# Kernel optimization log

Hardware: AMD Instinct MI355X
Metric: run time of the kernel (lower is better)

## Reference

```python
import jax, jax.numpy as jnp
import numpy as np

N_NODES = 100000
N_EDGES = 1600000
D_IN = 128
D_OUT = 128


def setup_inputs() -> dict:
    key = jax.random.key(0)
    k1, k2, k3, k4, k5, k6 = jax.random.split(key, 6)
    x = jax.random.normal(k1, (N_NODES, D_IN), dtype=jnp.float32)
    row = jnp.sort(jax.random.randint(k2, (N_EDGES,), 0, N_NODES, dtype=jnp.int32))
    col = jax.random.randint(k3, (N_EDGES,), 0, N_NODES, dtype=jnp.int32)
    val = jax.random.uniform(k4, (N_EDGES,), dtype=jnp.float32)
    # Glorot init for the two linear weights (stored as [in, out] for x @ W)
    std_l = float(np.sqrt(6.0 / (D_IN + D_OUT)))
    W_l = jax.random.uniform(k5, (D_IN, D_OUT), minval=-std_l, maxval=std_l, dtype=jnp.float32)
    b_l = jnp.zeros((D_OUT,), dtype=jnp.float32)
    W_r = jax.random.uniform(k6, (D_IN, D_OUT), minval=-std_l, maxval=std_l, dtype=jnp.float32)
    return {"x": x, "row": row, "col": col, "val": val, "W_l": W_l, "b_l": b_l, "W_r": W_r}


def reference(x, row, col, val, W_l, b_l, W_r):
    n = x.shape[0]
    # out_l = graph @ x  (sparse COO matmul: gather source feats, scale, scatter-add to rows)
    msg = val[:, None] * x[col]                      # [E, D_in]
    out_l = jax.ops.segment_sum(msg, row, num_segments=n)  # [N, D_in]
    # lin_l(out_l) + lin_r(x)
    return out_l @ W_l + b_l + x @ W_r
```

## Files before the change

kernel.cpp:

```cpp
#include <hip/hip_runtime.h>

#define D 128
typedef unsigned int uint32;
typedef __bf16 bf16x8 __attribute__((ext_vector_type(8)));
typedef float f32x4 __attribute__((ext_vector_type(4)));

__device__ __forceinline__ unsigned short f2bf(float f) {
    unsigned u = __float_as_uint(f);
    unsigned r = u + 0x7FFFu + ((u >> 16) & 1u);
    return (unsigned short)(r >> 16);
}
__device__ __forceinline__ float bflo(uint32 u) { return __uint_as_float(u << 16); }
__device__ __forceinline__ float bfhi(uint32 u) { return __uint_as_float(u & 0xFFFF0000u); }

__device__ __forceinline__ void fma8(float* acc, uint4 r, float v) {
    acc[0] += v * bflo(r.x); acc[1] += v * bfhi(r.x);
    acc[2] += v * bflo(r.y); acc[3] += v * bfhi(r.y);
    acc[4] += v * bflo(r.z); acc[5] += v * bfhi(r.z);
    acc[6] += v * bflo(r.w); acc[7] += v * bfhi(r.w);
}

__global__ __launch_bounds__(256) void prep_kernel(
    const float* __restrict__ x, unsigned short* __restrict__ xh, int n8,
    const int* __restrict__ row, int* __restrict__ row_ptr,
    int n_nodes, int n_edges,
    const float* __restrict__ Wl, const float* __restrict__ Wr,
    unsigned short* __restrict__ Wlt, unsigned short* __restrict__ Wrt,
    int nbConv, int nbRp) {
    const int b = blockIdx.x;
    if (b < nbConv) {
        const int id = b * 256 + threadIdx.x;
        if (id < n8) {
            const float4* p = (const float4*)x + (size_t)id * 2;
            float4 a = p[0], bb = p[1];
            uint4 o;
            o.x = f2bf(a.x) | ((uint32)f2bf(a.y) << 16);
            o.y = f2bf(a.z) | ((uint32)f2bf(a.w) << 16);
            o.z = f2bf(bb.x) | ((uint32)f2bf(bb.y) << 16);
            o.w = f2bf(bb.z) | ((uint32)f2bf(bb.w) << 16);
            ((uint4*)xh)[id] = o;
        }
    } else if (b < nbConv + nbRp) {
        const int e = (b - nbConv) * 256 + threadIdx.x;
        if (e < n_edges) {
            const int r = row[e];
            const int rp = (e == 0) ? -1 : row[e - 1];
            for (int n = rp + 1; n <= r; ++n) row_ptr[n] = e;
            if (e == n_edges - 1)
                for (int n = r + 1; n <= n_nodes; ++n) row_ptr[n] = n_edges;
        }
    } else {
        const int id = (b - nbConv - nbRp) * 256 + threadIdx.x;
        if (id < 16384) {
            const int n = id & 127, k = id >> 7;
            Wlt[n * 128 + k] = f2bf(Wl[k * 128 + n]);
            Wrt[n * 128 + k] = f2bf(Wr[k * 128 + n]);
        }
    }
}

__global__ __launch_bounds__(256) void spmm_bf16_kernel(
    const unsigned short* __restrict__ xh,
    const int* __restrict__ row_ptr,
    const int* __restrict__ col,
    const float* __restrict__ val,
    unsigned short* __restrict__ outlh, int n_nodes) {
    const int wid = threadIdx.x >> 6;
    const int n = blockIdx.x * 4 + wid;
    if (n >= n_nodes) return;
    const int lane = threadIdx.x & 63;
    const int g = lane >> 4;
    const int q8 = (lane & 15) * 8;

    const int start = row_ptr[n];
    const int end = row_ptr[n + 1];

    float acc[8] = {0.f, 0.f, 0.f, 0.f, 0.f, 0.f, 0.f, 0.f};

    int i = start + g;
    for (; i + 12 < end; i += 16) {
        const int c0 = col[i];      const float v0 = val[i];
        const int c1 = col[i + 4];  const float v1 = val[i + 4];
        const int c2 = col[i + 8];  const float v2 = val[i + 8];
        const int c3 = col[i + 12]; const float v3 = val[i + 12];
        const uint4 r0 = *(const uint4*)&xh[c0 * D + q8];
        const uint4 r1 = *(const uint4*)&xh[c1 * D + q8];
        const uint4 r2 = *(const uint4*)&xh[c2 * D + q8];
        const uint4 r3 = *(const uint4*)&xh[c3 * D + q8];
        fma8(acc, r0, v0);
        fma8(acc, r1, v1);
        fma8(acc, r2, v2);
        fma8(acc, r3, v3);
    }
    int c = 0; float v = 0.f;
    if (i < end) { c = col[i]; v = val[i]; }
    while (i < end) {
        const int i2 = i + 4;
        int c2 = 0; float v2 = 0.f;
        if (i2 < end) { c2 = col[i2]; v2 = val[i2]; }
        const uint4 r = *(const uint4*)&xh[c * D + q8];
        fma8(acc, r, v);
        i = i2; c = c2; v = v2;
    }
#pragma unroll
    for (int j = 0; j < 8; ++j) {
        acc[j] += __shfl_xor(acc[j], 16, 64);
        acc[j] += __shfl_xor(acc[j], 32, 64);
    }
    if (g == 0) {
        uint4 o;
        o.x = f2bf(acc[0]) | ((uint32)f2bf(acc[1]) << 16);
        o.y = f2bf(acc[2]) | ((uint32)f2bf(acc[3]) << 16);
        o.z = f2bf(acc[4]) | ((uint32)f2bf(acc[5]) << 16);
        o.w = f2bf(acc[6]) | ((uint32)f2bf(acc[7]) << 16);
        *(uint4*)&outlh[n * D + q8] = o;
    }
}

__global__ __launch_bounds__(256) void gemm_mfma_kernel(
    const unsigned short* __restrict__ xh,
    const unsigned short* __restrict__ outlh,
    const unsigned short* __restrict__ Wlt,
    const unsigned short* __restrict__ Wrt,
    const float* __restrict__ b_l,
    float* __restrict__ out, int M) {
    const int tid = threadIdx.x;
    const int wid = tid >> 6, lane = tid & 63;
    const int wm = wid >> 1, wn = wid & 1;
    const int m0 = blockIdx.x * 64 + wm * 32;
    const int n0 = wn * 64;
    const int fr = lane & 15;
    const int kofs = (lane >> 4) * 8;

    f32x4 acc[2][4];
#pragma unroll
    for (int mr = 0; mr < 2; ++mr)
#pragma unroll
        for (int nr = 0; nr < 4; ++nr) acc[mr][nr] = (f32x4){0.f, 0.f, 0.f, 0.f};

#pragma unroll
    for (int s = 0; s < 8; ++s) {
        const unsigned short* Abase = (s < 4) ? outlh : xh;
        const unsigned short* Wbase = (s < 4) ? Wlt : Wrt;
        const int k0 = (s & 3) * 32;
        bf16x8 a[2], b[4];
#pragma unroll
        for (int mr = 0; mr < 2; ++mr)
            a[mr] = *(const bf16x8*)&Abase[(m0 + mr * 16 + fr) * D + k0 + kofs];
#pragma unroll
        for (int nr = 0; nr < 4; ++nr)
            b[nr] = *(const bf16x8*)&Wbase[(n0 + nr * 16 + fr) * D + k0 + kofs];
#pragma unroll
        for (int mr = 0; mr < 2; ++mr)
#pragma unroll
            for (int nr = 0; nr < 4; ++nr)
                acc[mr][nr] = __builtin_amdgcn_mfma_f32_16x16x32_bf16(
                    a[mr], b[nr], acc[mr][nr], 0, 0, 0);
    }

    const int r0 = (lane >> 4) * 4;
#pragma unroll
    for (int nr = 0; nr < 4; ++nr) {
        const int ncol = n0 + nr * 16 + fr;
        const float bias = b_l[ncol];
#pragma unroll
        for (int mr = 0; mr < 2; ++mr) {
#pragma unroll
            for (int j = 0; j < 4; ++j) {
                const int m = m0 + mr * 16 + r0 + j;
                if (m < M) out[m * D + ncol] = acc[mr][nr][j] + bias;
            }
        }
    }
}

__global__ void build_rowptr_kernel(const int* __restrict__ row,
                                    int* __restrict__ row_ptr,
                                    int n_nodes, int n_edges) {
    int e = blockIdx.x * blockDim.x + threadIdx.x;
    if (e >= n_edges) return;
    int r = row[e];
    int rp = (e == 0) ? -1 : row[e - 1];
    for (int n = rp + 1; n <= r; ++n) row_ptr[n] = e;
    if (e == n_edges - 1)
        for (int n = r + 1; n <= n_nodes; ++n) row_ptr[n] = n_edges;
}

__global__ __launch_bounds__(128) void spmm_kernel(
    const float* __restrict__ x, const int* __restrict__ row_ptr,
    const int* __restrict__ col, const float* __restrict__ val,
    float* __restrict__ out_l) {
    const int n = blockIdx.x;
    const int d = threadIdx.x;
    const int start = row_ptr[n];
    const int end = row_ptr[n + 1];
    float acc = 0.0f;
    for (int e = start; e < end; ++e)
        acc += val[e] * x[(size_t)col[e] * D + d];
    out_l[(size_t)n * D + d] = acc;
}

__global__ __launch_bounds__(256) void fused_gemm_kernel(
    const float* __restrict__ xin, const float* __restrict__ W_l,
    const float* __restrict__ b_l, const float* __restrict__ W_r,
    float* __restrict__ out, int M) {
    __shared__ float As[64][68];
    __shared__ float Ws[64][132];
    const int tid = threadIdx.x;
    const int tx = tid & 15;
    const int ty = tid >> 4;
    const int ty4 = ty * 4;
    const int m0 = blockIdx.x * 64;
    float acc[4][8];
#pragma unroll
    for (int i = 0; i < 4; ++i)
#pragma unroll
        for (int j = 0; j < 8; ++j) acc[i][j] = 0.0f;
    for (int kt = 0; kt < 4; ++kt) {
        const float* Asrc = (kt < 2) ? out : xin;
        const float* Wsrc = (kt < 2) ? W_l : W_r;
        const int koff = (kt & 1) * 64;
        __syncthreads();
#pragma unroll
        for (int r = 0; r < 4; ++r) {
            const int idx = tid + r * 256;
            const int m = idx >> 4;
            const int kq = idx & 15;
            float4 a = make_float4(0.f, 0.f, 0.f, 0.f);
            if (m0 + m < M)
                a = *(const float4*)&Asrc[(size_t)(m0 + m) * D + koff + kq * 4];
            *(float4*)&As[m][kq * 4] = a;
        }
#pragma unroll
        for (int r = 0; r < 8; ++r) {
            const int idx = tid + r * 256;
            const int k = idx >> 5;
            const int j4 = idx & 31;
            *(float4*)&Ws[k][j4 * 4] =
                *(const float4*)&Wsrc[(size_t)(koff + k) * D + j4 * 4];
        }
        __syncthreads();
#pragma unroll 4
        for (int k = 0; k < 64; ++k) {
            const float a0 = As[ty4 + 0][k], a1 = As[ty4 + 1][k];
            const float a2 = As[ty4 + 2][k], a3 = As[ty4 + 3][k];
            const float4 w0 = *(const float4*)&Ws[k][tx * 4];
            const float4 w1 = *(const float4*)&Ws[k][64 + tx * 4];
            acc[0][0] += a0 * w0.x; acc[0][1] += a0 * w0.y; acc[0][2] += a0 * w0.z; acc[0][3] += a0 * w0.w;
            acc[0][4] += a0 * w1.x; acc[0][5] += a0 * w1.y; acc[0][6] += a0 * w1.z; acc[0][7] += a0 * w1.w;
            acc[1][0] += a1 * w0.x; acc[1][1] += a1 * w0.y; acc[1][2] += a1 * w0.z; acc[1][3] += a1 * w0.w;
            acc[1][4] += a1 * w1.x; acc[1][5] += a1 * w1.y; acc[1][6] += a1 * w1.z; acc[1][7] += a1 * w1.w;
            acc[2][0] += a2 * w0.x; acc[2][1] += a2 * w0.y; acc[2][2] += a2 * w0.z; acc[2][3] += a2 * w0.w;
            acc[2][4] += a2 * w1.x; acc[2][5] += a2 * w1.y; acc[2][6] += a2 * w1.z; acc[2][7] += a2 * w1.w;
            acc[3][0] += a3 * w0.x; acc[3][1] += a3 * w0.y; acc[3][2] += a3 * w0.z; acc[3][3] += a3 * w0.w;
            acc[3][4] += a3 * w1.x; acc[3][5] += a3 * w1.y; acc[3][6] += a3 * w1.z; acc[3][7] += a3 * w1.w;
        }
    }
    const float4 bv0 = *(const float4*)&b_l[tx * 4];
    const float4 bv1 = *(const float4*)&b_l[64 + tx * 4];
#pragma unroll
    for (int i = 0; i < 4; ++i) {
        const int m = m0 + ty4 + i;
        if (m < M) {
            float4 o0, o1;
            o0.x = acc[i][0] + bv0.x; o0.y = acc[i][1] + bv0.y;
            o0.z = acc[i][2] + bv0.z; o0.w = acc[i][3] + bv0.w;
            o1.x = acc[i][4] + bv1.x; o1.y = acc[i][5] + bv1.y;
            o1.z = acc[i][6] + bv1.z; o1.w = acc[i][7] + bv1.w;
            *(float4*)&out[(size_t)m * D + tx * 4] = o0;
            *(float4*)&out[(size_t)m * D + 64 + tx * 4] = o1;
        }
    }
}

static inline size_t align256(size_t x) { return (x + 255) & ~(size_t)255; }

extern "C" void kernel_launch(void* const* d_in, const int* in_sizes, int n_in,
                              void* d_out, int out_size, void* d_ws, size_t ws_size,
                              hipStream_t stream) {
    const float* x   = (const float*)d_in[0];
    const int*   row = (const int*)d_in[1];
    const int*   col = (const int*)d_in[2];
    const float* val = (const float*)d_in[3];
    const float* W_l = (const float*)d_in[4];
    const float* b_l = (const float*)d_in[5];
    const float* W_r = (const float*)d_in[6];
    float* out = (float*)d_out;

    const int n_nodes = in_sizes[0] / D;
    const int n_edges = in_sizes[1];

    const size_t xh_bytes   = (size_t)n_nodes * D * 2;
    const size_t outl_bytes = (size_t)n_nodes * D * 2;
    const size_t wt_bytes   = (size_t)D * D * 2;
    const size_t rp_bytes   = (size_t)(n_nodes + 1) * 4;
    size_t off = 0;
    const size_t xh_off   = off; off += align256(xh_bytes);
    const size_t outl_off = off; off += align256(outl_bytes);
    const size_t wlt_off  = off; off += align256(wt_bytes);
    const size_t wrt_off  = off; off += align256(wt_bytes);
    const size_t rp_off   = off; off += align256(rp_bytes);
    const size_t needed   = off + 65536;

    if (ws_size >= needed) {
        unsigned short* xh    = (unsigned short*)((char*)d_ws + xh_off);
        unsigned short* outlh = (unsigned short*)((char*)d_ws + outl_off);
        unsigned short* Wlt   = (unsigned short*)((char*)d_ws + wlt_off);
        unsigned short* Wrt   = (unsigned short*)((char*)d_ws + wrt_off);
        int* row_ptr          = (int*)((char*)d_ws + rp_off);

        const int n8 = n_nodes * D / 8;
        const int nbConv = (n8 + 255) / 256;
        const int nbRp   = (n_edges + 255) / 256;
        const int nbW    = 64;
        prep_kernel<<<nbConv + nbRp + nbW, 256, 0, stream>>>(
            x, xh, n8, row, row_ptr, n_nodes, n_edges,
            W_l, W_r, Wlt, Wrt, nbConv, nbRp);
        spmm_bf16_kernel<<<(n_nodes + 3) / 4, 256, 0, stream>>>(
            xh, row_ptr, col, val, outlh, n_nodes);
        gemm_mfma_kernel<<<(n_nodes + 63) / 64, 256, 0, stream>>>(
            xh, outlh, Wlt, Wrt, b_l, out, n_nodes);
    } else {
        int* row_ptr = (int*)d_ws;
        build_rowptr_kernel<<<(n_edges + 255) / 256, 256, 0, stream>>>(
            row, row_ptr, n_nodes, n_edges);
        spmm_kernel<<<n_nodes, 128, 0, stream>>>(x, row_ptr, col, val, out);
        fused_gemm_kernel<<<(n_nodes + 63) / 64, 256, 0, stream>>>(
            x, W_l, b_l, W_r, out, n_nodes);
    }
}
```

Baseline: 125.2 us.

## Stage block edge lists in LDS and map one 16-lane group per row

The SpMM kernel now handles 16 rows per block. The block first copies the contiguous col/val range for those rows into shared memory, with a global-memory fallback past a 1024-edge cap. Each 16-lane quarter-wave owns one row, so the cross-group shuffle reduction is gone, and a software-pipelined loop prefetches the next four gathered x rows while accumulating the current four. The aim is coalesced index loads and more independent gathers in flight, at the cost of a block-wide barrier and more imbalance across lanes when rows have uneven degrees.

```diff
diff --git a/kernel.cpp b/kernel.cpp
--- a/kernel.cpp
+++ b/kernel.cpp
@@ -1,6 +1,7 @@
 #include <hip/hip_runtime.h>
 
 #define D 128
+#define EDGE_CAP 1024
 typedef unsigned int uint32;
 typedef __bf16 bf16x8 __attribute__((ext_vector_type(8)));
 typedef float f32x4 __attribute__((ext_vector_type(4)));
@@ -65,49 +66,65 @@
     const int* __restrict__ col,
     const float* __restrict__ val,
     unsigned short* __restrict__ outlh, int n_nodes) {
-    const int wid = threadIdx.x >> 6;
-    const int n = blockIdx.x * 4 + wid;
-    if (n >= n_nodes) return;
-    const int lane = threadIdx.x & 63;
-    const int g = lane >> 4;
-    const int q8 = (lane & 15) * 8;
-
-    const int start = row_ptr[n];
-    const int end = row_ptr[n + 1];
+    __shared__ int   sc[EDGE_CAP];
+    __shared__ float sv[EDGE_CAP];
+    const int tid = threadIdx.x;
+    const int n0 = blockIdx.x * 16;
+    const int e0 = row_ptr[n0];
+    const int e1 = row_ptr[min(n0 + 16, n_nodes)];
+    const int ne = min(e1 - e0, EDGE_CAP);
+    for (int t = tid; t < ne; t += 256) {
+        sc[t] = col[e0 + t];
+        sv[t] = val[e0 + t];
+    }
+    __syncthreads();
+
+    const int wv = tid >> 6, lane = tid & 63;
+    const int g = lane >> 4, lq = lane & 15;
+    const int n = n0 + wv * 4 + g;
+    const int q8 = lq * 8;
+
+    int s = 0, e = 0;
+    if (n < n_nodes) { s = row_ptr[n]; e = row_ptr[n + 1]; }
 
     float acc[8] = {0.f, 0.f, 0.f, 0.f, 0.f, 0.f, 0.f, 0.f};
 
-    int i = start + g;
-    for (; i + 12 < end; i += 16) {
-        const int c0 = col[i];      const float v0 = val[i];
-        const int c1 = col[i + 4];  const float v1 = val[i + 4];
-        const int c2 = col[i + 8];  const float v2 = val[i + 8];
-        const int c3 = col[i + 12]; const float v3 = val[i + 12];
-        const uint4 r0 = *(const uint4*)&xh[c0 * D + q8];
-        const uint4 r1 = *(const uint4*)&xh[c1 * D + q8];
-        const uint4 r2 = *(const uint4*)&xh[c2 * D + q8];
-        const uint4 r3 = *(const uint4*)&xh[c3 * D + q8];
+    auto fetch = [&](int idx, int& c, float& v) {
+        if (idx < e) {
+            const int li = idx - e0;
+            if (li < EDGE_CAP) { c = sc[li]; v = sv[li]; }
+            else               { c = col[idx]; v = val[idx]; }
+        } else { c = 0; v = 0.f; }
+    };
+
+    int i = s;
+    int c0, c1, c2, c3; float v0, v1, v2, v3;
+    fetch(i + 0, c0, v0); fetch(i + 1, c1, v1);
+    fetch(i + 2, c2, v2); fetch(i + 3, c3, v3);
+    uint4 r0 = *(const uint4*)&xh[c0 * D + q8];
+    uint4 r1 = *(const uint4*)&xh[c1 * D + q8];
+    uint4 r2 = *(const uint4*)&xh[c2 * D + q8];
+    uint4 r3 = *(const uint4*)&xh[c3 * D + q8];
+
+    while (i < e) {
+        const int i2 = i + 4;
+        int d0, d1, d2, d3; float w0, w1, w2, w3;
+        fetch(i2 + 0, d0, w0); fetch(i2 + 1, d1, w1);
+        fetch(i2 + 2, d2, w2); fetch(i2 + 3, d3, w3);
+        const uint4 t0 = *(const uint4*)&xh[d0 * D + q8];
+        const uint4 t1 = *(const uint4*)&xh[d1 * D + q8];
+        const uint4 t2 = *(const uint4*)&xh[d2 * D + q8];
+        const uint4 t3 = *(const uint4*)&xh[d3 * D + q8];
         fma8(acc, r0, v0);
         fma8(acc, r1, v1);
         fma8(acc, r2, v2);
         fma8(acc, r3, v3);
-    }
-    int c = 0; float v = 0.f;
-    if (i < end) { c = col[i]; v = val[i]; }
-    while (i < end) {
-        const int i2 = i + 4;
-        int c2 = 0; float v2 = 0.f;
-        if (i2 < end) { c2 = col[i2]; v2 = val[i2]; }
-        const uint4 r = *(const uint4*)&xh[c * D + q8];
-        fma8(acc, r, v);
-        i = i2; c = c2; v = v2;
-    }
-#pragma unroll
-    for (int j = 0; j < 8; ++j) {
-        acc[j] += __shfl_xor(acc[j], 16, 64);
-        acc[j] += __shfl_xor(acc[j], 32, 64);
-    }
-    if (g == 0) {
+        r0 = t0; r1 = t1; r2 = t2; r3 = t3;
+        v0 = w0; v1 = w1; v2 = w2; v3 = w3;
+        i = i2;
+    }
+
+    if (n < n_nodes) {
         uint4 o;
         o.x = f2bf(acc[0]) | ((uint32)f2bf(acc[1]) << 16);
         o.y = f2bf(acc[2]) | ((uint32)f2bf(acc[3]) << 16);
@@ -316,7 +333,7 @@
         prep_kernel<<<nbConv + nbRp + nbW, 256, 0, stream>>>(
             x, xh, n8, row, row_ptr, n_nodes, n_edges,
             W_l, W_r, Wlt, Wrt, nbConv, nbRp);
-        spmm_bf16_kernel<<<(n_nodes + 3) / 4, 256, 0, stream>>>(
+        spmm_bf16_kernel<<<(n_nodes + 15) / 16, 256, 0, stream>>>(
             xh, row_ptr, col, val, outlh, n_nodes);
         gemm_mfma_kernel<<<(n_nodes + 63) / 64, 256, 0, stream>>>(
             xh, outlh, Wlt, Wrt, b_l, out, n_nodes);
```

After: 125.1 us. No clear change (-0.1%).
